# Optimization experiments

Measured on AMD Instinct MI355X. Metric: run time of the kernel, lower is better.

Reference implementation:

```python
import jax, jax.numpy as jnp
import numpy as np

B, L, D, H, R = 2, 2048, 1024, 16, 32
DH = D // H
LORA_SCALE = 64.0 / 32.0  # alpha / rank


def _ln(x, w, b):
    mu = jnp.mean(x, axis=-1, keepdims=True)
    xc = x - mu
    var = jnp.mean(xc * xc, axis=-1, keepdims=True)
    y = xc * jax.lax.rsqrt(var + 1e-5) * w
    return y + b if b is not None else y


def _rotate_half(x):
    x1, x2 = jnp.split(x, 2, axis=-1)
    return jnp.concatenate([-x2, x1], axis=-1)


def _apply_rotary(q, k):
    # q, k: [B, L, H, DH]
    seqlen = q.shape[1]
    inv_freq = 1.0 / (10000.0 ** (jnp.arange(0, DH, 2, dtype=jnp.float32) / DH))
    t = jnp.arange(seqlen, dtype=jnp.float32)
    freqs = t[:, None] * inv_freq[None, :]           # [L, DH/2]
    emb = jnp.concatenate([freqs, freqs], axis=-1)   # [L, DH]
    cos = jnp.cos(emb)[None, :, None, :]
    sin = jnp.sin(emb)[None, :, None, :]
    q = q * cos + _rotate_half(q) * sin
    k = k * cos + _rotate_half(k) * sin
    return q, k


def setup_inputs() -> dict:
    key = jax.random.key(0)
    ks = jax.random.split(key, 10)
    s = 0.02
    return {
        "x": jax.random.normal(ks[0], (B, L, D), dtype=jnp.float32),
        "seq_id": jnp.sort(jax.random.randint(ks[1], (B, L), 0, 4), axis=-1),
        "ln_w": jnp.ones((D,), jnp.float32),
        "ln_b": jnp.zeros((D,), jnp.float32),
        "w_qkv": jax.random.normal(ks[2], (3 * D, D), jnp.float32) * s,
        "q_lora_a": jax.random.normal(ks[3], (R, D), jnp.float32) * s,
        "q_lora_b": jax.random.normal(ks[4], (D, R), jnp.float32) * s,
        "v_lora_a": jax.random.normal(ks[5], (R, D), jnp.float32) * s,
        "v_lora_b": jax.random.normal(ks[6], (D, R), jnp.float32) * s,
        "q_ln_w": jnp.ones((D,), jnp.float32),
        "k_ln_w": jnp.ones((D,), jnp.float32),
        "w_out": jax.random.normal(ks[7], (D, D), jnp.float32) * s,
    }


def reference(x, seq_id, ln_w, ln_b, w_qkv, q_lora_a, q_lora_b,
              v_lora_a, v_lora_b, q_ln_w, k_ln_w, w_out):
    h = _ln(x, ln_w, ln_b)                          # [B, L, D]
    qkv = jnp.einsum('bld,ed->ble', h, w_qkv)       # [B, L, 3D]
    q, k, v = jnp.split(qkv, 3, axis=-1)
    q = q + LORA_SCALE * jnp.einsum('blr,dr->bld', jnp.einsum('bld,rd->blr', h, q_lora_a), q_lora_b)
    v = v + LORA_SCALE * jnp.einsum('blr,dr->bld', jnp.einsum('bld,rd->blr', h, v_lora_a), v_lora_b)
    q = _ln(q, q_ln_w, None)
    k = _ln(k, k_ln_w, None)
    q = q.reshape(B, L, H, DH)
    k = k.reshape(B, L, H, DH)
    q, k = _apply_rotary(q, k)
    qh = q.transpose(0, 2, 1, 3)                    # [B, H, L, DH]
    kh = k.transpose(0, 2, 1, 3)
    vh = v.reshape(B, L, H, DH).transpose(0, 2, 1, 3)
    scale = 1.0 / np.sqrt(DH)
    scores = jnp.einsum('bhqd,bhkd->bhqk', qh, kh) * scale
    mask = (seq_id[:, None, :, None] == seq_id[:, None, None, :])  # [B,1,L,L]
    scores = jnp.where(mask, scores, jnp.finfo(scores.dtype).min)
    attn = jax.nn.softmax(scores, axis=-1)
    ctx = jnp.einsum('bhqk,bhkd->bhqd', attn, vh)   # [B, H, L, DH]
    ctx = ctx.transpose(0, 2, 1, 3).reshape(B, L, D)
    return jnp.einsum('bld,ed->ble', ctx, w_out)
```

## Files before the change

### kernel.cpp

```cpp
#include <hip/hip_runtime.h>
#include <hip/hip_bf16.h>
#include <cmath>

constexpr int Bb = 2;
constexpr int Ls = 2048;
constexpr int Dd = 1024;
constexpr int Hh = 16;
constexpr int DHh = 64;
constexpr int Rr = 32;
constexpr int BL = Bb * Ls;
constexpr float LORA_SCALE = 2.0f;
constexpr float LN_EPS = 1e-5f;
constexpr float ATTN_SCALE = 0.125f;
constexpr float LOG2E = 1.4426950408889634f;
constexpr float QSCL = ATTN_SCALE * LOG2E;

typedef __attribute__((ext_vector_type(8))) short bf16x8;
typedef __attribute__((ext_vector_type(4))) float f32x4;

__device__ __forceinline__ unsigned short f2bf(float f) {
    __hip_bfloat16 b = __float2bfloat16(f);
    return *reinterpret_cast<unsigned short*>(&b);
}
__device__ __forceinline__ float bf2f(unsigned short u) {
    unsigned int x = ((unsigned int)u) << 16;
    return __uint_as_float(x);
}
__device__ __forceinline__ void async_copy16(const void* g, void* l) {
    __builtin_amdgcn_global_load_lds(
        (__attribute__((address_space(1))) void*)(void*)(size_t)g,
        (__attribute__((address_space(3))) void*)l, 16, 0, 0);
}

__device__ __forceinline__ float block_sum_256(float v, float* red) {
#pragma unroll
    for (int o = 32; o > 0; o >>= 1) v += __shfl_down(v, o, 64);
    const int lane = threadIdx.x & 63;
    const int wid = threadIdx.x >> 6;
    if (lane == 0) red[wid] = v;
    __syncthreads();
    float s = red[0] + red[1] + red[2] + red[3];
    __syncthreads();
    return s;
}

__global__ __launch_bounds__(256) void prep_kernel(const float* __restrict__ w,
                                                   const float* __restrict__ qa,
                                                   const float* __restrict__ qb,
                                                   const float* __restrict__ va,
                                                   const float* __restrict__ vb,
                                                   const float* __restrict__ wout,
                                                   unsigned short* __restrict__ wqkvb,
                                                   unsigned short* __restrict__ woutb,
                                                   float* __restrict__ ropec,
                                                   float* __restrict__ ropes) {
    const int blk = blockIdx.x;
    const int tid = threadIdx.x;
    if (blk < 3 * Dd) {
        const int e = blk;
        const int d0 = tid * 4;
        __shared__ float br[Rr];
        const bool isq = (e < Dd);
        const bool isv = (e >= 2 * Dd);
        const float* bsrc = isq ? (qb + (size_t)e * Rr)
                                : (isv ? (vb + (size_t)(e - 2 * Dd) * Rr) : nullptr);
        const float* asrc = isq ? qa : va;
        if (bsrc && tid < Rr) br[tid] = bsrc[tid];
        __syncthreads();
        float acc[4] = {0.f, 0.f, 0.f, 0.f};
        if (bsrc) {
#pragma unroll 8
            for (int r = 0; r < Rr; ++r) {
                float4 av = *(const float4*)(asrc + (size_t)r * Dd + d0);
                acc[0] += br[r] * av.x; acc[1] += br[r] * av.y;
                acc[2] += br[r] * av.z; acc[3] += br[r] * av.w;
            }
        }
        float4 wv = *(const float4*)(w + (size_t)e * Dd + d0);
        ushort4 o;
        o.x = f2bf(wv.x + LORA_SCALE * acc[0]);
        o.y = f2bf(wv.y + LORA_SCALE * acc[1]);
        o.z = f2bf(wv.z + LORA_SCALE * acc[2]);
        o.w = f2bf(wv.w + LORA_SCALE * acc[3]);
        *(ushort4*)(wqkvb + (size_t)e * Dd + d0) = o;
    } else if (blk < 4 * Dd) {
        int i = ((blk - 3 * Dd) * 256 + tid) * 4;
        float4 v = *(const float4*)(wout + i);
        ushort4 o;
        o.x = f2bf(v.x); o.y = f2bf(v.y); o.z = f2bf(v.z); o.w = f2bf(v.w);
        *(ushort4*)(woutb + i) = o;
    } else {
        int i = (blk - 4 * Dd) * 256 + tid;
        int l = i >> 5;
        int f = i & 31;
        float invf = powf(10000.0f, -(float)f * (1.0f / 32.0f));
        float ang = (float)l * invf;
        float s, c;
        sincosf(ang, &s, &c);
        ropec[i] = c;
        ropes[i] = s;
    }
}

__global__ __launch_bounds__(256) void ln_x_kernel(const float* __restrict__ x,
                                                   const float* __restrict__ w,
                                                   const float* __restrict__ b,
                                                   unsigned short* __restrict__ hb) {
    const int row = blockIdx.x;
    const int tid = threadIdx.x;
    __shared__ float red[4];
    float4 xv = *(const float4*)(x + (size_t)row * Dd + tid * 4);
    float v[4] = {xv.x, xv.y, xv.z, xv.w};
    float s = v[0] + v[1] + v[2] + v[3];
    float mean = block_sum_256(s, red) * (1.0f / Dd);
    float sq = 0.f;
#pragma unroll
    for (int j = 0; j < 4; ++j) {
        v[j] -= mean;
        sq += v[j] * v[j];
    }
    float var = block_sum_256(sq, red) * (1.0f / Dd);
    float rs = rsqrtf(var + LN_EPS);
    ushort4 o;
    unsigned short* op = (unsigned short*)&o;
#pragma unroll
    for (int j = 0; j < 4; ++j) {
        int d = tid * 4 + j;
        op[j] = f2bf(v[j] * rs * w[d] + b[d]);
    }
    *(ushort4*)(hb + (size_t)row * Dd + tid * 4) = o;
}

template <bool OUT_BF16>
__global__ __launch_bounds__(256) void gemm_bt_mfma(const unsigned short* __restrict__ A,
                                                    const unsigned short* __restrict__ B,
                                                    void* __restrict__ Cv,
                                                    int M, int N, int K) {
    __shared__ short As[128 * 64];
    __shared__ short Bs[128 * 64];
    const int tid = threadIdx.x;
    const int w = tid >> 6, lane = tid & 63, quad = lane >> 4, l15 = lane & 15;
    const int m0 = blockIdx.y * 128, n0 = blockIdx.x * 128;
    const int wm = (w & 1) * 64, wn = (w >> 1) * 64;
    f32x4 acc[4][4];
#pragma unroll
    for (int i = 0; i < 4; ++i)
#pragma unroll
        for (int j = 0; j < 4; ++j) acc[i][j] = f32x4{0.f, 0.f, 0.f, 0.f};

    for (int k0 = 0; k0 < K; k0 += 64) {
#pragma unroll
        for (int j = 0; j < 4; ++j) {
            int c = tid + j * 256;
            int row = c >> 3;
            int jg = (c & 7) ^ (row & 7);
            async_copy16(A + (size_t)(m0 + row) * K + k0 + jg * 8, As + c * 8);
        }
#pragma unroll
        for (int j = 0; j < 4; ++j) {
            int c = tid + j * 256;
            int row = c >> 3;
            int jg = (c & 7) ^ (row & 7);
            async_copy16(B + (size_t)(n0 + row) * K + k0 + jg * 8, Bs + c * 8);
        }
        __syncthreads();
#pragma unroll
        for (int ks = 0; ks < 2; ++ks) {
            bf16x8 a[4], b[4];
#pragma unroll
            for (int mi = 0; mi < 4; ++mi) {
                int row = wm + mi * 16 + l15;
                int ch = (ks * 4 + quad) ^ (row & 7);
                a[mi] = *(const bf16x8*)&As[row * 64 + ch * 8];
            }
#pragma unroll
            for (int ni = 0; ni < 4; ++ni) {
                int row = wn + ni * 16 + l15;
                int ch = (ks * 4 + quad) ^ (row & 7);
                b[ni] = *(const bf16x8*)&Bs[row * 64 + ch * 8];
            }
#pragma unroll
            for (int mi = 0; mi < 4; ++mi)
#pragma unroll
                for (int ni = 0; ni < 4; ++ni)
                    acc[mi][ni] = __builtin_amdgcn_mfma_f32_16x16x32_bf16(a[mi], b[ni], acc[mi][ni], 0, 0, 0);
        }
        __syncthreads();
    }
    if (OUT_BF16) {
        unsigned short* C = (unsigned short*)Cv;
#pragma unroll
        for (int mi = 0; mi < 4; ++mi)
#pragma unroll
            for (int ni = 0; ni < 4; ++ni)
#pragma unroll
                for (int r = 0; r < 4; ++r)
                    C[(size_t)(m0 + wm + mi * 16 + quad * 4 + r) * N + n0 + wn + ni * 16 + l15] =
                        f2bf(acc[mi][ni][r]);
    } else {
        float* C = (float*)Cv;
#pragma unroll
        for (int mi = 0; mi < 4; ++mi)
#pragma unroll
            for (int ni = 0; ni < 4; ++ni)
#pragma unroll
                for (int r = 0; r < 4; ++r)
                    C[(size_t)(m0 + wm + mi * 16 + quad * 4 + r) * N + n0 + wn + ni * 16 + l15] =
                        acc[mi][ni][r];
    }
}

__global__ __launch_bounds__(256) void qkv_final_kernel(const unsigned short* __restrict__ qkvb,
                                                        const float* __restrict__ qlnw,
                                                        const float* __restrict__ klnw,
                                                        const float* __restrict__ ropec,
                                                        const float* __restrict__ ropes,
                                                        unsigned short* __restrict__ qt,
                                                        unsigned short* __restrict__ kt) {
    const int row = blockIdx.x;
    const int b = row >> 11;
    const int l = row & (Ls - 1);
    const int tid = threadIdx.x;
    __shared__ float yrow[Dd];
    __shared__ float red[4];

    const int d0 = tid * 4;
    const int hh = d0 >> 6;
    const int dh0 = d0 & 63;
    float cs4[4], sn4[4];
#pragma unroll
    for (int j = 0; j < 4; ++j) {
        int f = (dh0 + j) & 31;
        cs4[j] = ropec[l * 32 + f];
        sn4[j] = ropes[l * 32 + f];
    }
    const size_t dst_off = (((size_t)(b * Hh + hh)) * Ls + l) * DHh + dh0;

    {
        ushort4 qv = *(const ushort4*)(qkvb + (size_t)row * (3 * Dd) + d0);
        float v[4] = {bf2f(qv.x), bf2f(qv.y), bf2f(qv.z), bf2f(qv.w)};
        float s = v[0] + v[1] + v[2] + v[3];
        float mean = block_sum_256(s, red) * (1.0f / Dd);
        float sq = 0.f;
#pragma unroll
        for (int j = 0; j < 4; ++j) {
            v[j] -= mean;
            sq += v[j] * v[j];
        }
        float var = block_sum_256(sq, red) * (1.0f / Dd);
        float rs = rsqrtf(var + LN_EPS);
#pragma unroll
        for (int j = 0; j < 4; ++j) yrow[d0 + j] = v[j] * rs * qlnw[d0 + j];
        __syncthreads();
        ushort4 pk;
        unsigned short* pp = (unsigned short*)&pk;
#pragma unroll
        for (int j = 0; j < 4; ++j) {
            int d = d0 + j;
            int dh = dh0 + j;
            float rot = (dh < 32) ? -yrow[d + 32] : yrow[d - 32];
            pp[j] = f2bf((yrow[d] * cs4[j] + rot * sn4[j]) * QSCL);
        }
        *(ushort4*)(qt + dst_off) = pk;
    }
    __syncthreads();

    {
        ushort4 kv = *(const ushort4*)(qkvb + (size_t)row * (3 * Dd) + Dd + d0);
        float v[4] = {bf2f(kv.x), bf2f(kv.y), bf2f(kv.z), bf2f(kv.w)};
        float s = v[0] + v[1] + v[2] + v[3];
        float mean = block_sum_256(s, red) * (1.0f / Dd);
        float sq = 0.f;
#pragma unroll
        for (int j = 0; j < 4; ++j) {
            v[j] -= mean;
            sq += v[j] * v[j];
        }
        float var = block_sum_256(sq, red) * (1.0f / Dd);
        float rs = rsqrtf(var + LN_EPS);
#pragma unroll
        for (int j = 0; j < 4; ++j) yrow[d0 + j] = v[j] * rs * klnw[d0 + j];
        __syncthreads();
        ushort4 pk;
        unsigned short* pp = (unsigned short*)&pk;
#pragma unroll
        for (int j = 0; j < 4; ++j) {
            int d = d0 + j;
            int dh = dh0 + j;
            float rot = (dh < 32) ? -yrow[d + 32] : yrow[d - 32];
            pp[j] = f2bf(yrow[d] * cs4[j] + rot * sn4[j]);
        }
        *(ushort4*)(kt + dst_off) = pk;
    }
}

__global__ __launch_bounds__(256) void transpose_v_kernel(const unsigned short* __restrict__ qkvb,
                                                          unsigned short* __restrict__ vtt) {
    const int l0 = blockIdx.x * 64;
    const int h = blockIdx.y;
    const int b = blockIdx.z;
    const int tid = threadIdx.x;
    __shared__ short t[64][72];
    const unsigned short* src = qkvb + (size_t)b * Ls * (3 * Dd) + 2 * Dd + h * 64;
#pragma unroll
    for (int j = 0; j < 2; ++j) {
        int g = tid + j * 256;
        int row = g >> 3;
        int c0 = (g & 7) * 8;
        uint4 vv = *(const uint4*)(src + (size_t)(l0 + row) * (3 * Dd) + c0);
        *(uint4*)&t[row][c0] = vv;
    }
    __syncthreads();
    unsigned short* dst = vtt + ((size_t)(b * Hh + h) * DHh) * Ls;
#pragma unroll
    for (int j = 0; j < 2; ++j) {
        int g = tid + j * 256;
        int dh = g >> 3;
        int lc = (g & 7) * 8;
        ushort4 o0, o1;
        unsigned short* p0 = (unsigned short*)&o0;
        unsigned short* p1 = (unsigned short*)&o1;
#pragma unroll
        for (int i = 0; i < 4; ++i) p0[i] = (unsigned short)t[lc + i][dh];
#pragma unroll
        for (int i = 0; i < 4; ++i) p1[i] = (unsigned short)t[lc + 4 + i][dh];
        *(ushort4*)(dst + (size_t)dh * Ls + l0 + lc) = o0;
        *(ushort4*)(dst + (size_t)dh * Ls + l0 + lc + 4) = o1;
    }
}

constexpr int PSP = 76;

__global__ __launch_bounds__(256) void attn_kernel(const unsigned short* __restrict__ qt,
                                                   const unsigned short* __restrict__ kt,
                                                   const unsigned short* __restrict__ vtt,
                                                   const int* __restrict__ seq_id,
                                                   unsigned short* __restrict__ ctxb) {
    const int id = blockIdx.x;
    const int c8 = id & 7;
    const int x = (id >> 3) & 31;
    const int g8 = id >> 8;
    const int v = c8 + 8 * g8;
    const int b = v >> 4;
    const int h = v & 15;
    const int q0 = x * 64;

    const size_t base = ((size_t)(b * Hh + h)) * Ls * DHh;
    const size_t base_v = ((size_t)(b * Hh + h)) * DHh * Ls;
    const int* sid = seq_id + (size_t)b * Ls;

    __shared__ short Qs[64 * 64];
    __shared__ short Ks[2][64 * 64];
    __shared__ short Vs[2][64 * 64];
    __shared__ short Ps[4][16 * PSP];
    __shared__ int sq_s[64];

    const int tid = threadIdx.x;
    const int w = tid >> 6;
    const int lane = tid & 63;
    const int quad = lane >> 4;
    const int l15 = lane & 15;

#pragma unroll
    for (int j = 0; j < 2; ++j) {
        int cc = tid + j * 256;
        int row = cc >> 3;
        int jg = (cc & 7) ^ (row & 7);
        async_copy16(qt + base + (size_t)(q0 + row) * DHh + jg * 8, Qs + cc * 8);
    }
    if (tid < 64) sq_s[tid] = sid[q0 + tid];
    const int qmin = sid[q0];
    const int qmax = sid[q0 + 63];

    bool need = false;
    if (lane < 32) {
        int kmn = sid[lane * 64];
        int kmx = sid[lane * 64 + 63];
        need = (kmn <= qmax) && (kmx >= qmin);
    }
    unsigned long long bmask = __ballot(need);
    const int t0 = __builtin_ctzll(bmask);
    const int t1 = 64 - __builtin_clzll(bmask);

    auto stage = [&](int t, int buf) {
        int k0 = t * 64;
#pragma unroll
        for (int j = 0; j < 2; ++j) {
            int cc = tid + j * 256;
            int row = cc >> 3;
            int jg = (cc & 7) ^ (row & 7);
            async_copy16(kt + base + (size_t)(k0 + row) * DHh + jg * 8, &Ks[buf][cc * 8]);
            async_copy16(vtt + base_v + (size_t)row * Ls + k0 + jg * 8, &Vs[buf][cc * 8]);
        }
    };

    stage(t0, 0);
    __syncthreads();

    float lsum[4] = {0.f, 0.f, 0.f, 0.f};
    f32x4 O[4];
#pragma unroll
    for (int r = 0; r < 4; ++r) O[r] = f32x4{0.f, 0.f, 0.f, 0.f};

    const int qrow = w * 16 + l15;
    bf16x8 a0 = *(const bf16x8*)&Qs[qrow * 64 + ((0 + quad) ^ (qrow & 7)) * 8];
    bf16x8 a1 = *(const bf16x8*)&Qs[qrow * 64 + ((4 + quad) ^ (qrow & 7)) * 8];

    int cur = 0;
    for (int t = t0; t < t1; ++t) {
        const int k0 = t * 64;
        if (t + 1 < t1) stage(t + 1, cur ^ 1);

        f32x4 s[4];
#pragma unroll
        for (int kg = 0; kg < 4; ++kg) {
            int krow = kg * 16 + l15;
            bf16x8 b0 = *(const bf16x8*)&Ks[cur][krow * 64 + ((0 + quad) ^ (krow & 7)) * 8];
            bf16x8 b1 = *(const bf16x8*)&Ks[cur][krow * 64 + ((4 + quad) ^ (krow & 7)) * 8];
            f32x4 acc = {0.f, 0.f, 0.f, 0.f};
            acc = __builtin_amdgcn_mfma_f32_16x16x32_bf16(a0, b0, acc, 0, 0, 0);
            acc = __builtin_amdgcn_mfma_f32_16x16x32_bf16(a1, b1, acc, 0, 0, 0);
            s[kg] = acc;
        }
        const int kmn = sid[k0];
        const int kmx = sid[k0 + 63];
        const bool nomask = (kmn == kmx) && (qmin == qmax) && (kmn == qmin);
        if (!nomask) {
            int sqv[4];
#pragma unroll
            for (int r = 0; r < 4; ++r) sqv[r] = sq_s[w * 16 + quad * 4 + r];
#pragma unroll
            for (int kg = 0; kg < 4; ++kg) {
                int skv = sid[k0 + kg * 16 + l15];
#pragma unroll
                for (int r = 0; r < 4; ++r)
                    if (sqv[r] != skv) s[kg][r] = -3.0e38f;
            }
        }
#pragma unroll
        for (int kg = 0; kg < 4; ++kg)
#pragma unroll
            for (int r = 0; r < 4; ++r)
                s[kg][r] = __builtin_amdgcn_exp2f(s[kg][r]);
#pragma unroll
        for (int r = 0; r < 4; ++r)
            lsum[r] += s[0][r] + s[1][r] + s[2][r] + s[3][r];
#pragma unroll
        for (int kg = 0; kg < 4; ++kg)
#pragma unroll
            for (int r = 0; r < 4; ++r)
                Ps[w][(quad * 4 + r) * PSP + kg * 16 + l15] = (short)f2bf(s[kg][r]);
        bf16x8 pa0 = *(const bf16x8*)&Ps[w][l15 * PSP + quad * 8];
        bf16x8 pa1 = *(const bf16x8*)&Ps[w][l15 * PSP + 32 + quad * 8];
#pragma unroll
        for (int ng = 0; ng < 4; ++ng) {
            int vrow = ng * 16 + l15;
            bf16x8 vb0 = *(const bf16x8*)&Vs[cur][vrow * 64 + ((0 + quad) ^ (vrow & 7)) * 8];
            bf16x8 vb1 = *(const bf16x8*)&Vs[cur][vrow * 64 + ((4 + quad) ^ (vrow & 7)) * 8];
            O[ng] = __builtin_amdgcn_mfma_f32_16x16x32_bf16(pa0, vb0, O[ng], 0, 0, 0);
            O[ng] = __builtin_amdgcn_mfma_f32_16x16x32_bf16(pa1, vb1, O[ng], 0, 0, 0);
        }
        __syncthreads();
        cur ^= 1;
    }

#pragma unroll
    for (int off = 1; off < 16; off <<= 1)
#pragma unroll
        for (int r = 0; r < 4; ++r)
            lsum[r] += __shfl_xor(lsum[r], off, 64);
    float inv_l[4];
#pragma unroll
    for (int r = 0; r < 4; ++r) inv_l[r] = 1.0f / lsum[r];
#pragma unroll
    for (int ng = 0; ng < 4; ++ng)
#pragma unroll
        for (int r = 0; r < 4; ++r) {
            int q = q0 + w * 16 + quad * 4 + r;
            ctxb[((size_t)b * Ls + q) * Dd + h * DHh + ng * 16 + l15] = f2bf(O[ng][r] * inv_l[r]);
        }
}

extern "C" void kernel_launch(void* const* d_in, const int* in_sizes, int n_in,
                              void* d_out, int out_size, void* d_ws, size_t ws_size,
                              hipStream_t stream) {
    const float* x = (const float*)d_in[0];
    const int* seq_id = (const int*)d_in[1];
    const float* ln_w = (const float*)d_in[2];
    const float* ln_b = (const float*)d_in[3];
    const float* w_qkv = (const float*)d_in[4];
    const float* q_lora_a = (const float*)d_in[5];
    const float* q_lora_b = (const float*)d_in[6];
    const float* v_lora_a = (const float*)d_in[7];
    const float* v_lora_b = (const float*)d_in[8];
    const float* q_ln_w = (const float*)d_in[9];
    const float* k_ln_w = (const float*)d_in[10];
    const float* w_out = (const float*)d_in[11];
    float* out = (float*)d_out;

    const size_t SZ = (size_t)BL * Dd;
    float* p = (float*)d_ws;
    float* ropec = p;          p += (size_t)Ls * 32;
    float* ropes = p;          p += (size_t)Ls * 32;
    unsigned short* ub = (unsigned short*)p;
    unsigned short* qkvb = ub; ub += 3 * SZ;
    unsigned short* hb = ub;   ub += SZ;
    unsigned short* qt = ub;   ub += SZ;
    unsigned short* kt = ub;   ub += SZ;
    unsigned short* vtt = ub;  ub += SZ;
    unsigned short* ctxb = ub; ub += SZ;
    unsigned short* wqkvb = ub; ub += (size_t)3 * Dd * Dd;
    unsigned short* woutb = ub; ub += (size_t)Dd * Dd;

    prep_kernel<<<4 * Dd + 256, 256, 0, stream>>>(w_qkv, q_lora_a, q_lora_b,
                                                  v_lora_a, v_lora_b, w_out,
                                                  wqkvb, woutb, ropec, ropes);
    ln_x_kernel<<<BL, 256, 0, stream>>>(x, ln_w, ln_b, hb);
    {
        dim3 g(3 * Dd / 128, BL / 128);
        gemm_bt_mfma<true><<<g, 256, 0, stream>>>(hb, wqkvb, qkvb, BL, 3 * Dd, Dd);
    }
    qkv_final_kernel<<<BL, 256, 0, stream>>>(qkvb, q_ln_w, k_ln_w,
                                             ropec, ropes, qt, kt);
    {
        dim3 g(Ls / 64, Hh, Bb);
        transpose_v_kernel<<<g, 256, 0, stream>>>(qkvb, vtt);
    }
    attn_kernel<<<1024, 256, 0, stream>>>(qt, kt, vtt, seq_id, ctxb);
    {
        dim3 g(Dd / 128, BL / 128);
        gemm_bt_mfma<false><<<g, 256, 0, stream>>>(ctxb, woutb, out, BL, Dd, Dd);
    }
}
```

Before: 223.0 us.

## Single-buffer K/V tiles and load Q fragments directly from global

Removes the double-buffered K/V staging in the attention kernel and uses a single LDS buffer, with a sync before and after each tile load. Q fragments are now read straight from global memory into registers instead of being staged through shared memory. This cuts LDS use (helping occupancy) but drops the overlap of the next tile's load with compute, so the loop is exposed to memory latency.

Measured after the change: 224.0 us. About the same (+0.5%).

```diff
diff --git a/kernel.cpp b/kernel.cpp
--- a/kernel.cpp
+++ b/kernel.cpp
@@ -349,9 +349,8 @@
     const size_t base_v = ((size_t)(b * Hh + h)) * DHh * Ls;
     const int* sid = seq_id + (size_t)b * Ls;
 
-    __shared__ short Qs[64 * 64];
-    __shared__ short Ks[2][64 * 64];
-    __shared__ short Vs[2][64 * 64];
+    __shared__ short Ks[64 * 64];
+    __shared__ short Vs[64 * 64];
     __shared__ short Ps[4][16 * PSP];
     __shared__ int sq_s[64];
 
@@ -361,16 +360,13 @@
     const int quad = lane >> 4;
     const int l15 = lane & 15;
 
-#pragma unroll
-    for (int j = 0; j < 2; ++j) {
-        int cc = tid + j * 256;
-        int row = cc >> 3;
-        int jg = (cc & 7) ^ (row & 7);
-        async_copy16(qt + base + (size_t)(q0 + row) * DHh + jg * 8, Qs + cc * 8);
-    }
     if (tid < 64) sq_s[tid] = sid[q0 + tid];
     const int qmin = sid[q0];
     const int qmax = sid[q0 + 63];
+
+    const int qrow = q0 + w * 16 + l15;
+    bf16x8 a0 = *(const bf16x8*)(qt + base + (size_t)qrow * DHh + quad * 8);
+    bf16x8 a1 = *(const bf16x8*)(qt + base + (size_t)qrow * DHh + 32 + quad * 8);
 
     bool need = false;
     if (lane < 32) {
@@ -382,41 +378,30 @@
     const int t0 = __builtin_ctzll(bmask);
     const int t1 = 64 - __builtin_clzll(bmask);
 
-    auto stage = [&](int t, int buf) {
-        int k0 = t * 64;
+    float lsum[4] = {0.f, 0.f, 0.f, 0.f};
+    f32x4 O[4];
+#pragma unroll
+    for (int r = 0; r < 4; ++r) O[r] = f32x4{0.f, 0.f, 0.f, 0.f};
+
+    for (int t = t0; t < t1; ++t) {
+        const int k0 = t * 64;
+        __syncthreads();
 #pragma unroll
         for (int j = 0; j < 2; ++j) {
             int cc = tid + j * 256;
             int row = cc >> 3;
             int jg = (cc & 7) ^ (row & 7);
-            async_copy16(kt + base + (size_t)(k0 + row) * DHh + jg * 8, &Ks[buf][cc * 8]);
-            async_copy16(vtt + base_v + (size_t)row * Ls + k0 + jg * 8, &Vs[buf][cc * 8]);
-        }
-    };
-
-    stage(t0, 0);
-    __syncthreads();
-
-    float lsum[4] = {0.f, 0.f, 0.f, 0.f};
-    f32x4 O[4];
-#pragma unroll
-    for (int r = 0; r < 4; ++r) O[r] = f32x4{0.f, 0.f, 0.f, 0.f};
-
-    const int qrow = w * 16 + l15;
-    bf16x8 a0 = *(const bf16x8*)&Qs[qrow * 64 + ((0 + quad) ^ (qrow & 7)) * 8];
-    bf16x8 a1 = *(const bf16x8*)&Qs[qrow * 64 + ((4 + quad) ^ (qrow & 7)) * 8];
-
-    int cur = 0;
-    for (int t = t0; t < t1; ++t) {
-        const int k0 = t * 64;
-        if (t + 1 < t1) stage(t + 1, cur ^ 1);
+            async_copy16(kt + base + (size_t)(k0 + row) * DHh + jg * 8, &Ks[cc * 8]);
+            async_copy16(vtt + base_v + (size_t)row * Ls + k0 + jg * 8, &Vs[cc * 8]);
+        }
+        __syncthreads();
 
         f32x4 s[4];
 #pragma unroll
         for (int kg = 0; kg < 4; ++kg) {
             int krow = kg * 16 + l15;
-            bf16x8 b0 = *(const bf16x8*)&Ks[cur][krow * 64 + ((0 + quad) ^ (krow & 7)) * 8];
-            bf16x8 b1 = *(const bf16x8*)&Ks[cur][krow * 64 + ((4 + quad) ^ (krow & 7)) * 8];
+            bf16x8 b0 = *(const bf16x8*)&Ks[krow * 64 + ((0 + quad) ^ (krow & 7)) * 8];
+            bf16x8 b1 = *(const bf16x8*)&Ks[krow * 64 + ((4 + quad) ^ (krow & 7)) * 8];
             f32x4 acc = {0.f, 0.f, 0.f, 0.f};
             acc = __builtin_amdgcn_mfma_f32_16x16x32_bf16(a0, b0, acc, 0, 0, 0);
             acc = __builtin_amdgcn_mfma_f32_16x16x32_bf16(a1, b1, acc, 0, 0, 0);
@@ -455,13 +440,11 @@
 #pragma unroll
         for (int ng = 0; ng < 4; ++ng) {
             int vrow = ng * 16 + l15;
-            bf16x8 vb0 = *(const bf16x8*)&Vs[cur][vrow * 64 + ((0 + quad) ^ (vrow & 7)) * 8];
-            bf16x8 vb1 = *(const bf16x8*)&Vs[cur][vrow * 64 + ((4 + quad) ^ (vrow & 7)) * 8];
+            bf16x8 vb0 = *(const bf16x8*)&Vs[vrow * 64 + ((0 + quad) ^ (vrow & 7)) * 8];
+            bf16x8 vb1 = *(const bf16x8*)&Vs[vrow * 64 + ((4 + quad) ^ (vrow & 7)) * 8];
             O[ng] = __builtin_amdgcn_mfma_f32_16x16x32_bf16(pa0, vb0, O[ng], 0, 0, 0);
             O[ng] = __builtin_amdgcn_mfma_f32_16x16x32_bf16(pa1, vb1, O[ng], 0, 0, 0);
         }
-        __syncthreads();
-        cur ^= 1;
     }
 
 #pragma unroll
```
